# Performance work log

Hardware: AMD Instinct MI355X
Metric: run time of the kernel (lower is better)

## Reference

```python
import jax, jax.numpy as jnp
import numpy as np

KERNEL = 25
PAD = (KERNEL - 1) // 2  # 12
LN_EPS = 1e-5
CAP_FACTOR = 2.0
K_VALUE = 2


def _moving_avg(x):
    # x: [B, L, D]; Autoformer moving_avg: replicate-pad ends, avg-pool k=25 stride 1
    front = jnp.repeat(x[:, :1, :], PAD, axis=1)
    end = jnp.repeat(x[:, -1:, :], PAD, axis=1)
    xp = jnp.concatenate([front, x, end], axis=1)            # [B, L+2*PAD, D]
    cs = jnp.cumsum(xp, axis=1)
    cs = jnp.concatenate([jnp.zeros_like(cs[:, :1]), cs], axis=1)
    return (cs[:, KERNEL:] - cs[:, :-KERNEL]) / KERNEL        # [B, L, D]


def _layernorm(h, g, b):
    mu = jnp.mean(h, axis=-1, keepdims=True)
    d = h - mu
    var = jnp.mean(d * d, axis=-1, keepdims=True)
    return d * jax.lax.rsqrt(var + LN_EPS) * g + b


def setup_inputs() -> dict:
    key = jax.random.key(0)
    ks = jax.random.split(key, 6)
    B, L, D, H, E = 32, 512, 512, 1024, 8
    sd_in = 1.0 / np.sqrt(D)
    sd_h = 1.0 / np.sqrt(H)
    return {
        "x": jax.random.normal(ks[0], (B, L, D), jnp.float32),
        "Wt": jax.random.normal(ks[1], (D, H), jnp.float32) * sd_in,
        "bt": jax.random.normal(ks[2], (H,), jnp.float32) * sd_in,
        "gt": jnp.ones((H,), jnp.float32),
        "bet": jnp.zeros((H,), jnp.float32),
        "Ws": jax.random.normal(ks[3], (D, H), jnp.float32) * sd_in,
        "bs": jax.random.normal(ks[4], (H,), jnp.float32) * sd_in,
        "gs": jnp.ones((H,), jnp.float32),
        "bes": jnp.zeros((H,), jnp.float32),
        "W2": jax.random.normal(ks[5], (H, E), jnp.float32) * sd_h,
        "b2": jnp.zeros((E,), jnp.float32),
    }


def reference(x, Wt, bt, gt, bet, Ws, bs, gs, bes, W2, b2):
    # series decomposition: (residual, moving_mean) -> (trend_init, seasonal_init)
    ma = _moving_avg(x)
    trend_init = x - ma          # residual (first return of series_decomp)
    seasonal_init = ma           # moving mean (second return)

    t = _layernorm(trend_init @ Wt + bt, gt, bet)       # [B, L, H]
    s = _layernorm(seasonal_init @ Ws + bs, gs, bes)    # [B, L, H]
    med = jax.nn.relu(t + s)
    logits = med @ W2 + b2                               # [B, L, E]
    gate_scores = jax.nn.softmax(logits, axis=-1)

    B, L, E = gate_scores.shape
    capacity = int(CAP_FACTOR * B)

    _, top_k_indices = jax.lax.top_k(gate_scores, K_VALUE)  # [B, L, K]
    # torch scatter_(1, idx, 1) on 3D: mask[b, idx[b,l,j], j] = 1
    bi = jnp.arange(B)[:, None, None]
    ji = jnp.arange(K_VALUE)[None, None, :]
    mask = jnp.zeros_like(gate_scores).at[bi, top_k_indices, ji].set(1.0)

    masked = gate_scores * mask
    denom = jnp.sum(masked, axis=0, keepdims=True) + 1e-4    # [1, L, E]
    return masked / denom * capacity
```

## Files before the change

kernel.cpp:

```cpp
#include <hip/hip_runtime.h>

#define NB 32
#define NL 512
#define ND 512
#define NH 1024
#define NE 8
#define NROWS (NB * NL)
#define CW 2048
#define SPAD 136

typedef __attribute__((ext_vector_type(8))) short bf16x8;
typedef __attribute__((ext_vector_type(4))) float f32x4;
typedef __attribute__((ext_vector_type(4))) unsigned u32x4;

__device__ __forceinline__ unsigned short f2bf(float f) {
    unsigned u = __float_as_uint(f);
    return (unsigned short)((u + 0x7fffu + ((u >> 16) & 1u)) >> 16);
}
__device__ __forceinline__ float bf2f(unsigned short b) {
    return __uint_as_float(((unsigned)b) << 16);
}
__device__ __forceinline__ unsigned pktr(float a, float b) {
    return __builtin_amdgcn_perm(__float_as_uint(b), __float_as_uint(a), 0x07060302u);
}

__global__ __launch_bounds__(256) void wprep(
    const float* __restrict__ Wt, const float* __restrict__ Ws,
    unsigned* __restrict__ bpack)
{
    __shared__ float tile[64][65];
    int bid = blockIdx.x;
    int mat = bid >> 7, rem = bid & 127;
    int kt0 = (rem >> 4) << 6;
    int nt0 = (rem & 15) << 6;
    const float* W = mat ? Ws : Wt;
    unsigned* Oh = bpack;
    unsigned* Ol = bpack + 524288u;
    int t = threadIdx.x;
    #pragma unroll
    for (int i = 0; i < 16; ++i) {
        int idx = t + 256 * i;
        int k = idx >> 6, n = idx & 63;
        tile[k][n] = W[(size_t)(kt0 + k) * NH + nt0 + n];
    }
    __syncthreads();
    #pragma unroll
    for (int i = 0; i < 8; ++i) {
        int idx = t + 256 * i;
        int jp = idx & 3, lane = (idx >> 2) & 63, kbr = (idx >> 8) & 1, ntr = (idx >> 9) & 3;
        int ncol = ntr * 16 + (lane & 15);
        int kcol = kbr * 32 + ((lane >> 4) << 3) + jp * 2;
        float w0 = tile[kcol][ncol], w1 = tile[kcol + 1][ncol];
        unsigned short h0 = f2bf(w0), h1 = f2bf(w1);
        unsigned short l0 = f2bf(w0 - bf2f(h0)), l1 = f2bf(w1 - bf2f(h1));
        int ntg = mat * 64 + (nt0 >> 4) + ntr;
        int kb = (kt0 >> 5) + kbr;
        unsigned offs = ((unsigned)(ntg * 16 + kb) * 64u + (unsigned)lane) * 4u + jp;
        Oh[offs] = (unsigned)h0 | ((unsigned)h1 << 16);
        Ol[offs] = (unsigned)l0 | ((unsigned)l1 << 16);
    }
}

__global__ __launch_bounds__(256, 4) void gemm_all(
    const float* __restrict__ x, const unsigned* __restrict__ bpack,
    unsigned short* __restrict__ C, unsigned short* __restrict__ Clo)
{
    __shared__ union {
        unsigned short A[2][64][40];
        unsigned short cs[64][264];
    } sm;

    const int tid = threadIdx.x, lane = tid & 63, wave = tid >> 6;
    const int g = lane >> 4, c = lane & 15;

    if (blockIdx.x >= 256) {
        const int bid = blockIdx.x - 256;
        const int xcd = bid & 7, idx = bid >> 3;
        const int mi = xcd * 32 + (idx >> 3), ni = idx & 7;
        const int m0 = mi * 64;

        f32x4 acc[4][4];
        #pragma unroll
        for (int nf = 0; nf < 4; ++nf)
            #pragma unroll
            for (int mf = 0; mf < 4; ++mf) acc[nf][mf] = (f32x4){0.f, 0.f, 0.f, 0.f};

        const int srow = tid >> 2, sj = tid & 3;
        const float* xs = x + (size_t)(m0 + srow) * ND + sj * 8;

        auto loadB = [&](int kb2, int nf) -> bf16x8 {
            int nt = ni * 16 + wave * 4 + nf;
            return *(const bf16x8*)(bpack + ((size_t)(nt * 16 + kb2) * 64 + lane) * 4);
        };

        float4 xa = *(const float4*)xs;
        float4 xb = *(const float4*)(xs + 4);
        bf16x8 bc0 = loadB(0, 0), bc1 = loadB(0, 1), bc2 = loadB(0, 2), bc3 = loadB(0, 3);

        for (int kb = 0; kb < 16; ++kb) {
            const int p = kb & 1;
            u32x4 u;
            u.x = pktr(xa.x, xa.y); u.y = pktr(xa.z, xa.w);
            u.z = pktr(xb.x, xb.y); u.w = pktr(xb.z, xb.w);
            *(u32x4*)&sm.A[p][srow][sj * 8] = u;
            bf16x8 bn0, bn1, bn2, bn3;
            if (kb < 15) {
                const float* pn = xs + (kb + 1) * 32;
                xa = *(const float4*)pn;
                xb = *(const float4*)(pn + 4);
                bn0 = loadB(kb + 1, 0); bn1 = loadB(kb + 1, 1);
                bn2 = loadB(kb + 1, 2); bn3 = loadB(kb + 1, 3);
            }
            __syncthreads();

            bf16x8 af[4];
            #pragma unroll
            for (int mf = 0; mf < 4; ++mf)
                af[mf] = *(const bf16x8*)&sm.A[p][mf * 16 + c][g * 8];
            #pragma unroll
            for (int mf = 0; mf < 4; ++mf) {
                acc[0][mf] = __builtin_amdgcn_mfma_f32_16x16x32_bf16(af[mf], bc0, acc[0][mf], 0, 0, 0);
                acc[1][mf] = __builtin_amdgcn_mfma_f32_16x16x32_bf16(af[mf], bc1, acc[1][mf], 0, 0, 0);
                acc[2][mf] = __builtin_amdgcn_mfma_f32_16x16x32_bf16(af[mf], bc2, acc[2][mf], 0, 0, 0);
                acc[3][mf] = __builtin_amdgcn_mfma_f32_16x16x32_bf16(af[mf], bc3, acc[3][mf], 0, 0, 0);
            }
            if (kb < 15) { bc0 = bn0; bc1 = bn1; bc2 = bn2; bc3 = bn3; }
        }

        __syncthreads();
        #pragma unroll
        for (int nf = 0; nf < 4; ++nf)
            #pragma unroll
            for (int mf = 0; mf < 4; ++mf)
                #pragma unroll
                for (int r = 0; r < 4; ++r)
                    sm.cs[mf * 16 + g * 4 + r][wave * 64 + nf * 16 + c] =
                        (unsigned short)(__float_as_uint(acc[nf][mf][r]) >> 16);
        __syncthreads();
        #pragma unroll
        for (int i = 0; i < 8; ++i) {
            int idx2 = tid + 256 * i;
            int row = idx2 >> 5, cg = idx2 & 31;
            int grow = m0 + row;
            if ((grow & 511) >= 32)
                *(uint4*)&C[(size_t)grow * CW + ni * 256 + cg * 8] = *(const uint4*)&sm.cs[row][cg * 8];
        }
    } else {
        const int eb = blockIdx.x;
        const int bq = eb >> 3, ni = eb & 7;
        const int m0 = bq * NL;
        const unsigned* Bhi = bpack;
        const unsigned* Blo = bpack + 524288u;

        f32x4 acc[4][2];
        #pragma unroll
        for (int nf = 0; nf < 4; ++nf)
            #pragma unroll
            for (int mf = 0; mf < 2; ++mf) acc[nf][mf] = (f32x4){0.f, 0.f, 0.f, 0.f};

        const float* xr0 = x + (size_t)(m0 + c) * ND + g * 8;
        #pragma unroll 2
        for (int kb = 0; kb < 16; ++kb) {
            bf16x8 ah[2], al[2];
            #pragma unroll
            for (int mf = 0; mf < 2; ++mf) {
                const float* p = xr0 + mf * (16 * ND) + kb * 32;
                float4 a0 = *(const float4*)p;
                float4 a1 = *(const float4*)(p + 4);
                float f[8] = {a0.x, a0.y, a0.z, a0.w, a1.x, a1.y, a1.z, a1.w};
                float lo[8];
                #pragma unroll
                for (int j = 0; j < 8; ++j) {
                    float hif = __uint_as_float(__float_as_uint(f[j]) & 0xFFFF0000u);
                    lo[j] = f[j] - hif;
                }
                u32x4 uh, ul;
                uh.x = pktr(f[0], f[1]); uh.y = pktr(f[2], f[3]);
                uh.z = pktr(f[4], f[5]); uh.w = pktr(f[6], f[7]);
                ul.x = pktr(lo[0], lo[1]); ul.y = pktr(lo[2], lo[3]);
                ul.z = pktr(lo[4], lo[5]); ul.w = pktr(lo[6], lo[7]);
                ah[mf] = __builtin_bit_cast(bf16x8, uh);
                al[mf] = __builtin_bit_cast(bf16x8, ul);
            }
            #pragma unroll
            for (int nf = 0; nf < 4; ++nf) {
                int nt = ni * 16 + wave * 4 + nf;
                size_t bo = ((size_t)(nt * 16 + kb) * 64 + lane) * 4;
                bf16x8 bh = *(const bf16x8*)(Bhi + bo);
                bf16x8 bl = *(const bf16x8*)(Blo + bo);
                #pragma unroll
                for (int mf = 0; mf < 2; ++mf) {
                    acc[nf][mf] = __builtin_amdgcn_mfma_f32_16x16x32_bf16(ah[mf], bh, acc[nf][mf], 0, 0, 0);
                    acc[nf][mf] = __builtin_amdgcn_mfma_f32_16x16x32_bf16(al[mf], bh, acc[nf][mf], 0, 0, 0);
                    acc[nf][mf] = __builtin_amdgcn_mfma_f32_16x16x32_bf16(ah[mf], bl, acc[nf][mf], 0, 0, 0);
                }
            }
        }

        #pragma unroll
        for (int nf = 0; nf < 4; ++nf)
            #pragma unroll
            for (int mf = 0; mf < 2; ++mf)
                #pragma unroll
                for (int r = 0; r < 4; ++r)
                    sm.cs[mf * 16 + g * 4 + r][wave * 64 + nf * 16 + c] =
                        (unsigned short)(__float_as_uint(acc[nf][mf][r]) >> 16);
        __syncthreads();
        #pragma unroll
        for (int i = 0; i < 4; ++i) {
            int idx2 = tid + 256 * i;
            int row = idx2 >> 5, cg = idx2 & 31;
            *(uint4*)&C[(size_t)(m0 + row) * CW + ni * 256 + cg * 8] = *(const uint4*)&sm.cs[row][cg * 8];
        }
        __syncthreads();
        #pragma unroll
        for (int nf = 0; nf < 4; ++nf)
            #pragma unroll
            for (int mf = 0; mf < 2; ++mf)
                #pragma unroll
                for (int r = 0; r < 4; ++r) {
                    float v = acc[nf][mf][r];
                    float hif = __uint_as_float(__float_as_uint(v) & 0xFFFF0000u);
                    sm.cs[mf * 16 + g * 4 + r][wave * 64 + nf * 16 + c] =
                        (unsigned short)(__float_as_uint(v - hif) >> 16);
                }
        __syncthreads();
        #pragma unroll
        for (int i = 0; i < 3; ++i) {
            int idx2 = tid + 256 * i;
            int row = idx2 >> 5, cg = idx2 & 31;
            if (row < 20)
                *(uint4*)&Clo[((size_t)bq * 20 + row) * CW + ni * 256 + cg * 8] = *(const uint4*)&sm.cs[row][cg * 8];
        }
    }
}

__global__ __launch_bounds__(256) void stats_all(
    const unsigned short* __restrict__ C, const unsigned short* __restrict__ Clo,
    const float* __restrict__ bt, const float* __restrict__ bs,
    float* __restrict__ rowpart, float* __restrict__ exstat)
{
    __shared__ unsigned short stg[88][SPAD];
    const int tid = threadIdx.x;

    if (blockIdx.x < 1024) {
        const int bid = blockIdx.x;
        const int q = bid & 3, lc = (bid >> 2) & 7, b = bid >> 5;
        const int l0 = lc * 64;
        const int cq = tid & 31, rg = tid >> 5;
        const float inv25 = 1.f / 25.f;

        float s[8], qa[8];
        #pragma unroll
        for (int r = 0; r < 8; ++r) { s[r] = 0.f; qa[r] = 0.f; }

        for (int ch = 0; ch < 4; ++ch) {
            int cb = q * 512 + ch * 128;
            __syncthreads();
            for (int i = tid; i < 1408; i += 256) {
                int si = i >> 4, cg = i & 15;
                int gl = l0 - 12 + si;
                gl = gl < 0 ? 0 : (gl > NL - 1 ? NL - 1 : gl);
                *(uint4*)&stg[si][cg * 8] = *(const uint4*)&C[(size_t)(b * NL + gl) * CW + cb + cg * 8];
            }
            __syncthreads();

            float bv[4];
            {
                float4 b4 = q < 2 ? *(const float4*)&bt[cb + cq * 4]
                                  : *(const float4*)&bs[cb - 1024 + cq * 4];
                bv[0] = b4.x; bv[1] = b4.y; bv[2] = b4.z; bv[3] = b4.w;
            }
            float run[4] = {0.f, 0.f, 0.f, 0.f};
            #pragma unroll
            for (int w = 0; w < 25; ++w) {
                ushort4 u = *(const ushort4*)&stg[rg * 8 + w][cq * 4];
                run[0] += bf2f(u.x); run[1] += bf2f(u.y); run[2] += bf2f(u.z); run[3] += bf2f(u.w);
            }
            #pragma unroll
            for (int rr = 0; rr < 8; ++rr) {
                if (rr > 0) {
                    ushort4 un = *(const ushort4*)&stg[rg * 8 + rr + 24][cq * 4];
                    ushort4 uo = *(const ushort4*)&stg[rg * 8 + rr - 1][cq * 4];
                    run[0] += bf2f(un.x) - bf2f(uo.x); run[1] += bf2f(un.y) - bf2f(uo.y);
                    run[2] += bf2f(un.z) - bf2f(uo.z); run[3] += bf2f(un.w) - bf2f(uo.w);
                }
                float pre[4];
                if (q < 2) {
                    ushort4 uc = *(const ushort4*)&stg[rg * 8 + rr + 12][cq * 4];
                    pre[0] = bf2f(uc.x) - run[0] * inv25 + bv[0];
                    pre[1] = bf2f(uc.y) - run[1] * inv25 + bv[1];
                    pre[2] = bf2f(uc.z) - run[2] * inv25 + bv[2];
                    pre[3] = bf2f(uc.w) - run[3] * inv25 + bv[3];
                } else {
                    pre[0] = run[0] * inv25 + bv[0];
                    pre[1] = run[1] * inv25 + bv[1];
                    pre[2] = run[2] * inv25 + bv[2];
                    pre[3] = run[3] * inv25 + bv[3];
                }
                s[rr]  += pre[0] + pre[1] + pre[2] + pre[3];
                qa[rr] += pre[0] * pre[0] + pre[1] * pre[1] + pre[2] * pre[2] + pre[3] * pre[3];
            }
        }

        #pragma unroll
        for (int rr = 0; rr < 8; ++rr)
            #pragma unroll
            for (int o = 1; o < 32; o <<= 1) {
                s[rr]  += __shfl_xor(s[rr], o);
                qa[rr] += __shfl_xor(qa[rr], o);
            }
        if (cq == 0) {
            #pragma unroll
            for (int rr = 0; rr < 8; ++rr) {
                size_t gr = (size_t)b * NL + l0 + rg * 8 + rr;
                rowpart[(gr * 4 + q) * 2 + 0] = s[rr];
                rowpart[(gr * 4 + q) * 2 + 1] = qa[rr];
            }
        }
    } else {
        const int inst = (blockIdx.x - 1024) * 4 + (tid >> 6);
        const int b = inst >> 3, chunk = inst & 7;
        const int t = tid & 63;
        const int c4 = chunk * 256 + t * 4;
        const bool isU = chunk < 4;
        const float inv25 = 1.f / 25.f;

        float bias[4];
        {
            float4 b4 = isU ? *(const float4*)&bt[c4] : *(const float4*)&bs[c4 - 1024];
            bias[0] = b4.x; bias[1] = b4.y; bias[2] = b4.z; bias[3] = b4.w;
        }
        float s[8], q[8];
        #pragma unroll
        for (int r = 0; r < 8; ++r) { s[r] = 0.f; q[r] = 0.f; }

        float cs2[4] = {0, 0, 0, 0}, v0[4], keep[8][4];
        #pragma unroll
        for (int j = 0; j < 20; ++j) {
            ushort4 h  = *(const ushort4*)&C[(size_t)(b * NL + j) * CW + c4];
            ushort4 lo = *(const ushort4*)&Clo[((size_t)b * 20 + j) * CW + c4];
            float u[4] = {bf2f(h.x) + bf2f(lo.x), bf2f(h.y) + bf2f(lo.y),
                          bf2f(h.z) + bf2f(lo.z), bf2f(h.w) + bf2f(lo.w)};
            if (j == 0) {
                #pragma unroll
                for (int k = 0; k < 4; ++k) v0[k] = u[k];
            }
            if (j < 8) {
                #pragma unroll
                for (int k = 0; k < 4; ++k) keep[j][k] = u[k];
            }
            #pragma unroll
            for (int k = 0; k < 4; ++k) cs2[k] += u[k];
            if (j >= 12) {
                const int l = j - 12;
                const float w0 = (float)(24 - j);
                #pragma unroll
                for (int k = 0; k < 4; ++k) {
                    float ma = (cs2[k] + w0 * v0[k]) * inv25;
                    float pre = isU ? (keep[l][k] - ma + bias[k]) : (ma + bias[k]);
                    s[l] += pre;
                    q[l] += pre * pre;
                }
            }
        }
        #pragma unroll
        for (int r = 0; r < 8; ++r)
            #pragma unroll
            for (int o = 1; o < 64; o <<= 1) {
                s[r] += __shfl_xor(s[r], o);
                q[r] += __shfl_xor(q[r], o);
            }
        if (t == 0) {
            #pragma unroll
            for (int r = 0; r < 8; ++r) {
                exstat[(((size_t)b * 8 + chunk) * 8 + r) * 2 + 0] = s[r];
                exstat[(((size_t)b * 8 + chunk) * 8 + r) * 2 + 1] = q[r];
            }
        }
    }
}

__global__ __launch_bounds__(64) void exact_apply(
    const unsigned short* __restrict__ C, const unsigned short* __restrict__ Clo,
    const float* __restrict__ bt, const float* __restrict__ gt, const float* __restrict__ bet,
    const float* __restrict__ bs, const float* __restrict__ gs, const float* __restrict__ bes,
    const float* __restrict__ W2, const float* __restrict__ exstat,
    float* __restrict__ exlg)
{
    const int t = threadIdx.x;
    const int chunk = blockIdx.x & 7, b = blockIdx.x >> 3;
    const int h2 = chunk * 128 + t * 2;
    const float inv25 = 1.f / 25.f;

    float mu_t[8], rs_t[8], mu_s[8], rs_s[8];
    #pragma unroll
    for (int l = 0; l < 8; ++l) {
        float st = 0.f, qt = 0.f, ss = 0.f, qs = 0.f;
        #pragma unroll
        for (int ch = 0; ch < 4; ++ch) {
            st += exstat[(((size_t)b * 8 + ch) * 8 + l) * 2 + 0];
            qt += exstat[(((size_t)b * 8 + ch) * 8 + l) * 2 + 1];
            ss += exstat[(((size_t)b * 8 + 4 + ch) * 8 + l) * 2 + 0];
            qs += exstat[(((size_t)b * 8 + 4 + ch) * 8 + l) * 2 + 1];
        }
        mu_t[l] = st * (1.f / NH);
        rs_t[l] = rsqrtf(qt * (1.f / NH) - mu_t[l] * mu_t[l] + 1e-5f);
        mu_s[l] = ss * (1.f / NH);
        rs_s[l] = rsqrtf(qs * (1.f / NH) - mu_s[l] * mu_s[l] + 1e-5f);
    }

    float btv[2], gtv[2], bev[2], bsv[2], gsv[2], besv[2], w2r[2][NE];
    #pragma unroll
    for (int k = 0; k < 2; ++k) {
        int h = h2 + k;
        btv[k] = bt[h]; gtv[k] = gt[h]; bev[k] = bet[h];
        bsv[k] = bs[h]; gsv[k] = gs[h]; besv[k] = bes[h];
        const float4* wp = (const float4*)&W2[(size_t)h * NE];
        float4 a = wp[0], c2 = wp[1];
        w2r[k][0] = a.x;  w2r[k][1] = a.y;  w2r[k][2] = a.z;  w2r[k][3] = a.w;
        w2r[k][4] = c2.x; w2r[k][5] = c2.y; w2r[k][6] = c2.z; w2r[k][7] = c2.w;
    }

    float csU[2] = {0, 0}, csV[2] = {0, 0}, v0U[2], v0V[2], keepU[8][2];
    float lg[8][NE];
    #pragma unroll
    for (int l = 0; l < 8; ++l)
        #pragma unroll
        for (int e = 0; e < NE; ++e) lg[l][e] = 0.f;

    #pragma unroll
    for (int j = 0; j < 20; ++j) {
        size_t rb = (size_t)(b * NL + j) * CW;
        size_t lb = ((size_t)b * 20 + j) * CW;
        ushort2 hu  = *(const ushort2*)&C[rb + h2];
        ushort2 lu  = *(const ushort2*)&Clo[lb + h2];
        ushort2 hv  = *(const ushort2*)&C[rb + NH + h2];
        ushort2 lv  = *(const ushort2*)&Clo[lb + NH + h2];
        float u[2] = {bf2f(hu.x) + bf2f(lu.x), bf2f(hu.y) + bf2f(lu.y)};
        float v[2] = {bf2f(hv.x) + bf2f(lv.x), bf2f(hv.y) + bf2f(lv.y)};
        if (j == 0) {
            #pragma unroll
            for (int k = 0; k < 2; ++k) { v0U[k] = u[k]; v0V[k] = v[k]; }
        }
        if (j < 8) {
            #pragma unroll
            for (int k = 0; k < 2; ++k) keepU[j][k] = u[k];
        }
        #pragma unroll
        for (int k = 0; k < 2; ++k) { csU[k] += u[k]; csV[k] += v[k]; }
        if (j >= 12) {
            const int l = j - 12;
            const float w0 = (float)(24 - j);
            #pragma unroll
            for (int k = 0; k < 2; ++k) {
                float maU = (csU[k] + w0 * v0U[k]) * inv25;
                float maV = (csV[k] + w0 * v0V[k]) * inv25;
                float tn = ((keepU[l][k] - maU + btv[k]) - mu_t[l]) * rs_t[l] * gtv[k] + bev[k];
                float sn = ((maV + bsv[k]) - mu_s[l]) * rs_s[l] * gsv[k] + besv[k];
                float m = tn + sn; m = m > 0.f ? m : 0.f;
                #pragma unroll
                for (int e = 0; e < NE; ++e) lg[l][e] = fmaf(m, w2r[k][e], lg[l][e]);
            }
        }
    }
    #pragma unroll
    for (int l = 0; l < 8; ++l)
        #pragma unroll
        for (int e = 0; e < NE; ++e)
            #pragma unroll
            for (int o = 1; o < 64; o <<= 1)
                lg[l][e] += __shfl_xor(lg[l][e], o);
    if (t == 0) {
        #pragma unroll
        for (int l = 0; l < 8; ++l)
            #pragma unroll
            for (int e = 0; e < NE; ++e)
                exlg[(((size_t)b * 8 + chunk) * 8 + l) * NE + e] = lg[l][e];
    }
}

__global__ __launch_bounds__(256) void apply_k(
    const unsigned short* __restrict__ C,
    const float* __restrict__ bt, const float* __restrict__ gt, const float* __restrict__ bet,
    const float* __restrict__ bs, const float* __restrict__ gs, const float* __restrict__ bes,
    const float* __restrict__ W2, const float* __restrict__ rowpart,
    float* __restrict__ lgpart)
{
    __shared__ unsigned short stgU[88][SPAD];
    __shared__ unsigned short stgV[88][SPAD];
    __shared__ float4 rowstat[64];

    const int tid = threadIdx.x;
    const int bid = blockIdx.x;
    const int q = bid & 3, lc = (bid >> 2) & 7, b = bid >> 5;
    const int l0 = lc * 64;
    const int cq = tid & 31, rg = tid >> 5;
    const float inv25 = 1.f / 25.f;

    if (tid < 64) {
        size_t gr = (size_t)b * NL + l0 + tid;
        const float* p = &rowpart[gr * 8];
        float st = p[0] + p[2], qt = p[1] + p[3];
        float ss = p[4] + p[6], qs = p[5] + p[7];
        float mut = st * (1.f / NH), mus = ss * (1.f / NH);
        float vt = qt * (1.f / NH) - mut * mut;
        float vs = qs * (1.f / NH) - mus * mus;
        rowstat[tid] = make_float4(mut, rsqrtf(vt + 1e-5f), mus, rsqrtf(vs + 1e-5f));
    }

    float lgp[8][NE];
    #pragma unroll
    for (int r = 0; r < 8; ++r)
        #pragma unroll
        for (int e = 0; e < NE; ++e) lgp[r][e] = 0.f;

    for (int ch = 0; ch < 2; ++ch) {
        int hb = q * 256 + ch * 128;
        __syncthreads();
        for (int i = tid; i < 1408; i += 256) {
            int si = i >> 4, cg = i & 15;
            int gl = l0 - 12 + si;
            gl = gl < 0 ? 0 : (gl > NL - 1 ? NL - 1 : gl);
            size_t rb = (size_t)(b * NL + gl) * CW;
            *(uint4*)&stgU[si][cg * 8] = *(const uint4*)&C[rb + hb + cg * 8];
            *(uint4*)&stgV[si][cg * 8] = *(const uint4*)&C[rb + NH + hb + cg * 8];
        }
        __syncthreads();

        int col = hb + cq * 4;
        float4 btv = *(const float4*)&bt[col],  gtv = *(const float4*)&gt[col];
        float4 bev = *(const float4*)&bet[col], bsv = *(const float4*)&bs[col];
        float4 gsv = *(const float4*)&gs[col],  besv = *(const float4*)&bes[col];
        float btr[4] = {btv.x, btv.y, btv.z, btv.w};
        float gtr[4] = {gtv.x, gtv.y, gtv.z, gtv.w};
        float ber[4] = {bev.x, bev.y, bev.z, bev.w};
        float bsr[4] = {bsv.x, bsv.y, bsv.z, bsv.w};
        float gsr[4] = {gsv.x, gsv.y, gsv.z, gsv.w};
        float besr[4] = {besv.x, besv.y, besv.z, besv.w};
        float w2r[4][NE];
        #pragma unroll
        for (int j = 0; j < 4; ++j) {
            const float4* wp = (const float4*)&W2[(size_t)(col + j) * NE];
            float4 a = wp[0], c2 = wp[1];
            w2r[j][0] = a.x;  w2r[j][1] = a.y;  w2r[j][2] = a.z;  w2r[j][3] = a.w;
            w2r[j][4] = c2.x; w2r[j][5] = c2.y; w2r[j][6] = c2.z; w2r[j][7] = c2.w;
        }

        float runU[4] = {0.f, 0.f, 0.f, 0.f}, runV[4] = {0.f, 0.f, 0.f, 0.f};
        #pragma unroll
        for (int w = 0; w < 25; ++w) {
            ushort4 u = *(const ushort4*)&stgU[rg * 8 + w][cq * 4];
            ushort4 v = *(const ushort4*)&stgV[rg * 8 + w][cq * 4];
            runU[0] += bf2f(u.x); runU[1] += bf2f(u.y); runU[2] += bf2f(u.z); runU[3] += bf2f(u.w);
            runV[0] += bf2f(v.x); runV[1] += bf2f(v.y); runV[2] += bf2f(v.z); runV[3] += bf2f(v.w);
        }
        #pragma unroll
        for (int rr = 0; rr < 8; ++rr) {
            if (rr > 0) {
                ushort4 un = *(const ushort4*)&stgU[rg * 8 + rr + 24][cq * 4];
                ushort4 uo = *(const ushort4*)&stgU[rg * 8 + rr - 1][cq * 4];
                ushort4 vn = *(const ushort4*)&stgV[rg * 8 + rr + 24][cq * 4];
                ushort4 vo = *(const ushort4*)&stgV[rg * 8 + rr - 1][cq * 4];
                runU[0] += bf2f(un.x) - bf2f(uo.x); runU[1] += bf2f(un.y) - bf2f(uo.y);
                runU[2] += bf2f(un.z) - bf2f(uo.z); runU[3] += bf2f(un.w) - bf2f(uo.w);
                runV[0] += bf2f(vn.x) - bf2f(vo.x); runV[1] += bf2f(vn.y) - bf2f(vo.y);
                runV[2] += bf2f(vn.z) - bf2f(vo.z); runV[3] += bf2f(vn.w) - bf2f(vo.w);
            }
            float4 rs = rowstat[rg * 8 + rr];
            ushort4 uc = *(const ushort4*)&stgU[rg * 8 + rr + 12][cq * 4];
            float cen[4] = {bf2f(uc.x), bf2f(uc.y), bf2f(uc.z), bf2f(uc.w)};
            float med[4];
            #pragma unroll
            for (int j = 0; j < 4; ++j) {
                float tn = ((cen[j] - runU[j] * inv25 + btr[j]) - rs.x) * rs.y * gtr[j] + ber[j];
                float sn = ((runV[j] * inv25 + bsr[j]) - rs.z) * rs.w * gsr[j] + besr[j];
                float m = tn + sn;
                med[j] = m > 0.f ? m : 0.f;
            }
            #pragma unroll
            for (int e = 0; e < NE; ++e)
                lgp[rr][e] = fmaf(med[0], w2r[0][e], fmaf(med[1], w2r[1][e],
                             fmaf(med[2], w2r[2][e], fmaf(med[3], w2r[3][e], lgp[rr][e]))));
        }
    }

    #pragma unroll
    for (int rr = 0; rr < 8; ++rr)
        #pragma unroll
        for (int e = 0; e < NE; ++e)
            #pragma unroll
            for (int o = 1; o < 32; o <<= 1)
                lgp[rr][e] += __shfl_xor(lgp[rr][e], o);
    if (cq == 0) {
        #pragma unroll
        for (int rr = 0; rr < 8; ++rr) {
            size_t gr = (size_t)b * NL + l0 + rg * 8 + rr;
            #pragma unroll
            for (int e = 0; e < NE; ++e)
                lgpart[(gr * 4 + q) * NE + e] = lgp[rr][e];
        }
    }
}

__global__ __launch_bounds__(256) void final_all(
    const float* __restrict__ lgpart, const float* __restrict__ exlg,
    const float* __restrict__ b2,
    unsigned* __restrict__ mb, float* __restrict__ gates)
{
    const int t = threadIdx.x;
    if (blockIdx.x < 64) {
        int row = blockIdx.x * 256 + t;
        int b = row >> 9, l = row & (NL - 1);
        float lg[NE];
        #pragma unroll
        for (int e = 0; e < NE; ++e) lg[e] = b2[e];
        #pragma unroll
        for (int qq = 0; qq < 4; ++qq)
            #pragma unroll
            for (int e = 0; e < NE; ++e)
                lg[e] += lgpart[((size_t)row * 4 + qq) * NE + e];
        int i0 = 0;
        #pragma unroll
        for (int e = 1; e < NE; ++e) if (lg[e] > lg[i0]) i0 = e;
        int i1 = i0 == 0 ? 1 : 0;
        #pragma unroll
        for (int e = 0; e < NE; ++e) if (e != i0 && lg[e] > lg[i1]) i1 = e;
        unsigned m = (l < 8) ? 0u : ((1u << i0) | (1u << (8 + i1)));
        #pragma unroll
        for (int o = 1; o < 64; o <<= 1) m |= __shfl_xor(m, o);
        if ((t & 63) == 0) {
            atomicOr(&mb[2 * b + 0], m & 0xffu);
            atomicOr(&mb[2 * b + 1], m >> 8);
        }
    } else {
        const int b = t >> 3, l = t & 7;
        float lg[NE];
        #pragma unroll
        for (int e = 0; e < NE; ++e) lg[e] = b2[e];
        #pragma unroll
        for (int ch = 0; ch < 8; ++ch)
            #pragma unroll
            for (int e = 0; e < NE; ++e)
                lg[e] += exlg[(((size_t)b * 8 + ch) * 8 + l) * NE + e];
        float mx = lg[0];
        #pragma unroll
        for (int e = 1; e < NE; ++e) mx = lg[e] > mx ? lg[e] : mx;
        float p[NE]; float sum = 0.f;
        #pragma unroll
        for (int e = 0; e < NE; ++e) { p[e] = expf(lg[e] - mx); sum += p[e]; }
        float inv = 1.f / sum;
        #pragma unroll
        for (int e = 0; e < NE; ++e)
            gates[((size_t)b * 8 + l) * NE + e] = p[e] * inv;
        int i0 = 0;
        #pragma unroll
        for (int e = 1; e < NE; ++e) if (lg[e] > lg[i0]) i0 = e;
        int i1 = i0 == 0 ? 1 : 0;
        #pragma unroll
        for (int e = 0; e < NE; ++e) if (e != i0 && lg[e] > lg[i1]) i1 = e;
        unsigned m = (1u << i0) | (1u << (8 + i1));
        m |= __shfl_xor(m, 1); m |= __shfl_xor(m, 2); m |= __shfl_xor(m, 4);
        if (l == 0) {
            atomicOr(&mb[2 * b + 0], m & 0xffu);
            atomicOr(&mb[2 * b + 1], m >> 8);
        }
    }
}

__global__ void finalize_k(const unsigned* __restrict__ mb,
                           const float* __restrict__ gates,
                           float* __restrict__ out)
{
    int t = threadIdx.x;
    if (t >= 16) return;
    int l = t >> 1, e = t & 1;
    float m[NB];
    float sum = 0.f;
    #pragma unroll
    for (int bb = 0; bb < NB; ++bb) {
        float gvv = gates[((size_t)bb * 8 + l) * NE + e];
        float on  = ((mb[2 * bb + e] >> l) & 1u) ? 1.f : 0.f;
        m[bb] = gvv * on;
        sum += m[bb];
    }
    float scale = 64.f / (sum + 1e-4f);
    #pragma unroll
    for (int bb = 0; bb < NB; ++bb)
        out[(size_t)bb * (NL * NE) + l * NE + e] = m[bb] * scale;
}

extern "C" void kernel_launch(void* const* d_in, const int* in_sizes, int n_in,
                              void* d_out, int out_size, void* d_ws, size_t ws_size,
                              hipStream_t stream) {
    const float* x   = (const float*)d_in[0];
    const float* Wt  = (const float*)d_in[1];
    const float* bt  = (const float*)d_in[2];
    const float* gt  = (const float*)d_in[3];
    const float* bet = (const float*)d_in[4];
    const float* Ws  = (const float*)d_in[5];
    const float* bs  = (const float*)d_in[6];
    const float* gs  = (const float*)d_in[7];
    const float* bes = (const float*)d_in[8];
    const float* W2  = (const float*)d_in[9];
    const float* b2  = (const float*)d_in[10];
    float* out = (float*)d_out;

    char* wsb = (char*)d_ws;
    unsigned*       mbp     = (unsigned*)wsb;
    float*          gates   = (float*)(wsb + 256);
    unsigned*       bpack   = (unsigned*)(wsb + 4096);
    float*          rowpart = (float*)(wsb + 4096);
    float*          lgpart  = (float*)(wsb + 4096 + 524288);
    float*          exstat  = (float*)(wsb + 4096 + 524288 + 2097152);
    float*          exlg    = (float*)(wsb + 4096 + 524288 + 2097152 + 16384);
    unsigned short* C       = (unsigned short*)(wsb + 4096 + 4194304);
    unsigned short* Clo     = (unsigned short*)(wsb + 4096 + 4194304 + (size_t)NROWS * CW * 2);

    hipMemsetAsync(d_out, 0, sizeof(float) * NB * NL * NE, stream);
    hipMemsetAsync(mbp, 0, 256, stream);

    wprep<<<256, 256, 0, stream>>>(Wt, Ws, bpack);
    gemm_all<<<2304, 256, 0, stream>>>(x, bpack, C, Clo);
    stats_all<<<1088, 256, 0, stream>>>(C, Clo, bt, bs, rowpart, exstat);
    exact_apply<<<256, 64, 0, stream>>>(C, Clo, bt, gt, bet, bs, gs, bes, W2, exstat, exlg);
    apply_k<<<1024, 256, 0, stream>>>(C, bt, gt, bet, bs, gs, bes, W2, rowpart, lgpart);
    final_all<<<65, 256, 0, stream>>>(lgpart, exlg, b2, mbp, gates);
    finalize_k<<<1, 64, 0, stream>>>(mbp, gates, out);
}
```

Before: 158.6 us.

## Give each wave a private LDS A tile and drop per-iteration block barriers

Each wave now loads and converts its own full copy of the 64x32 A slab into a private LDS buffer instead of sharing one block-wide double-buffered tile. This removes the __syncthreads inside the K loop and the explicit register prefetch of A and B, relying on unroll-by-2 and the compiler to overlap loads. The cost is four times the global A reads and bf16 conversion work per block, plus the loss of software prefetching, so loads may be exposed.

Result: slower. 195.3 us (+23.2%).

```diff
diff --git a/kernel.cpp b/kernel.cpp
--- a/kernel.cpp
+++ b/kernel.cpp
@@ -66,7 +66,7 @@
     unsigned short* __restrict__ C, unsigned short* __restrict__ Clo)
 {
     __shared__ union {
-        unsigned short A[2][64][40];
+        unsigned short A[4][64][40];
         unsigned short cs[64][264];
     } sm;
 
@@ -85,46 +85,37 @@
             #pragma unroll
             for (int mf = 0; mf < 4; ++mf) acc[nf][mf] = (f32x4){0.f, 0.f, 0.f, 0.f};
 
-        const int srow = tid >> 2, sj = tid & 3;
-        const float* xs = x + (size_t)(m0 + srow) * ND + sj * 8;
+        const int l4 = lane & 3, lr = lane >> 2;
+        const float* xs = x + (size_t)(m0 + lr) * ND + l4 * 8;
 
         auto loadB = [&](int kb2, int nf) -> bf16x8 {
             int nt = ni * 16 + wave * 4 + nf;
             return *(const bf16x8*)(bpack + ((size_t)(nt * 16 + kb2) * 64 + lane) * 4);
         };
 
-        float4 xa = *(const float4*)xs;
-        float4 xb = *(const float4*)(xs + 4);
-        bf16x8 bc0 = loadB(0, 0), bc1 = loadB(0, 1), bc2 = loadB(0, 2), bc3 = loadB(0, 3);
-
+        #pragma unroll 2
         for (int kb = 0; kb < 16; ++kb) {
-            const int p = kb & 1;
-            u32x4 u;
-            u.x = pktr(xa.x, xa.y); u.y = pktr(xa.z, xa.w);
-            u.z = pktr(xb.x, xb.y); u.w = pktr(xb.z, xb.w);
-            *(u32x4*)&sm.A[p][srow][sj * 8] = u;
-            bf16x8 bn0, bn1, bn2, bn3;
-            if (kb < 15) {
-                const float* pn = xs + (kb + 1) * 32;
-                xa = *(const float4*)pn;
-                xb = *(const float4*)(pn + 4);
-                bn0 = loadB(kb + 1, 0); bn1 = loadB(kb + 1, 1);
-                bn2 = loadB(kb + 1, 2); bn3 = loadB(kb + 1, 3);
-            }
-            __syncthreads();
-
+            #pragma unroll
+            for (int q = 0; q < 4; ++q) {
+                const float* src = xs + (size_t)(q * 16) * ND + kb * 32;
+                float4 a0 = *(const float4*)src;
+                float4 a1 = *(const float4*)(src + 4);
+                u32x4 u;
+                u.x = pktr(a0.x, a0.y); u.y = pktr(a0.z, a0.w);
+                u.z = pktr(a1.x, a1.y); u.w = pktr(a1.z, a1.w);
+                *(u32x4*)&sm.A[wave][q * 16 + lr][l4 * 8] = u;
+            }
             bf16x8 af[4];
             #pragma unroll
             for (int mf = 0; mf < 4; ++mf)
-                af[mf] = *(const bf16x8*)&sm.A[p][mf * 16 + c][g * 8];
-            #pragma unroll
-            for (int mf = 0; mf < 4; ++mf) {
-                acc[0][mf] = __builtin_amdgcn_mfma_f32_16x16x32_bf16(af[mf], bc0, acc[0][mf], 0, 0, 0);
-                acc[1][mf] = __builtin_amdgcn_mfma_f32_16x16x32_bf16(af[mf], bc1, acc[1][mf], 0, 0, 0);
-                acc[2][mf] = __builtin_amdgcn_mfma_f32_16x16x32_bf16(af[mf], bc2, acc[2][mf], 0, 0, 0);
-                acc[3][mf] = __builtin_amdgcn_mfma_f32_16x16x32_bf16(af[mf], bc3, acc[3][mf], 0, 0, 0);
-            }
-            if (kb < 15) { bc0 = bn0; bc1 = bn1; bc2 = bn2; bc3 = bn3; }
+                af[mf] = *(const bf16x8*)&sm.A[wave][mf * 16 + c][g * 8];
+            #pragma unroll
+            for (int nf = 0; nf < 4; ++nf) {
+                bf16x8 bfr = loadB(kb, nf);
+                #pragma unroll
+                for (int mf = 0; mf < 4; ++mf)
+                    acc[nf][mf] = __builtin_amdgcn_mfma_f32_16x16x32_bf16(af[mf], bfr, acc[nf][mf], 0, 0, 0);
+            }
         }
 
         __syncthreads();
```
